# Kernel tuning notes

Measured on AMD Instinct MI355X. Metric: run time of the kernel, lower is better.

The kernel has to match this reference:

```python
import jax
import jax.numpy as jnp
import numpy as np
from jax import lax

STD = 1.0          # prior gaussian std
LAMBDA_2 = 0.1
LAMBDA_3 = 1000.0
MAX_ITER = 20
TOL = 1e-05
DIM = 512
SEQ = 4096


def mahalanobis_dist(P, Q, M):
    # dist[i,j] = (P_i - Q_j)^T M (P_i - Q_j)
    pMp = jnp.einsum('id,de,ie->i', P, M, P)          # [m]
    qMq = jnp.einsum('jd,de,je->j', Q, M, Q)          # [n]
    cross = P @ (M + M.T) @ Q.T                        # [m,n]
    return pMp[:, None] + qMq[None, :] - cross


def sinkhorn_iterative(K, alpha, beta, max_iter=MAX_ITER, tol=TOL):
    # Faithful replication of the torch loop (check at iter%20==1 or iter==max_iter).
    ainvK = K / alpha
    KT = K.T

    def check(u, v, it):
        v2 = beta / (KT @ u)
        u2 = 1.0 / (ainvK @ v2)
        crit = jnp.max(jnp.abs(jnp.sum(jnp.abs(v2 * (KT @ u2) - beta), axis=0)))  # inf-norm
        return u2, v2, it + 1, jnp.abs(crit) < tol

    def cond(state):
        _, _, it, done = state
        return (it < max_iter) & (~done)

    def body(state):
        u, v, it, done = state
        u = 1.0 / (ainvK @ (beta / (KT @ u)))
        it = it + 1
        do_check = ((it % 20) == 1) | (it == max_iter)
        return lax.cond(do_check,
                        lambda: check(u, v, it),
                        lambda: (u, v, it, done))

    u0 = alpha
    v0 = jnp.zeros_like(beta)
    u, v, _, _ = lax.while_loop(cond, body,
                                (u0, v0, jnp.asarray(0, jnp.int32), jnp.asarray(False)))
    return u, v


def W_M(P, Q, M):
    m, n = P.shape[0], Q.shape[0]
    dtype = P.dtype
    dist = mahalanobis_dist(P, Q, M)                                  # [m,n]
    alpha = (jnp.arange(1, m + 1, dtype=dtype) / m)[:, None]          # [m,1]
    beta = (jnp.arange(1, n + 1, dtype=dtype) / n)[:, None]           # [n,1]
    rel = alpha - beta.T                                              # [m,n]
    denom = jnp.sqrt(1.0 / n**2 + 1.0 / m**2)
    prior = (1.0 / (STD * np.sqrt(2.0 * np.pi))) * jnp.exp(
        -(jnp.abs(rel) / denom) ** 2 / (2.0 * STD**2))
    K = prior * jnp.exp(-(dist - LAMBDA_2 / (rel**2 + 1.0)) / LAMBDA_3)
    Kng = lax.stop_gradient(K)                                        # torch computed K under no_grad
    u, v = sinkhorn_iterative(Kng, alpha, beta)
    F = lax.stop_gradient(u * Kng * v.T)                              # detached transport plan
    return jnp.sum(F * dist)


def setup_inputs() -> dict:
    key = jax.random.key(0)
    kP, kQ, kR, kS, kM = jax.random.split(key, 5)
    P = jax.random.normal(kP, (SEQ, DIM), dtype=jnp.float32)
    Q = jax.random.normal(kQ, (SEQ, DIM), dtype=jnp.float32)
    R = jax.random.normal(kR, (SEQ, DIM), dtype=jnp.float32)
    S = jax.random.normal(kS, (SEQ, DIM), dtype=jnp.float32)
    M = jax.random.normal(kM, (DIM, DIM), dtype=jnp.float32)          # learned metric parameter
    return {"P": P, "Q": Q, "R": R, "S": S, "M": M}


def reference(P, Q, R, S, M):
    return W_M(P, Q, M) - W_M(R, S, M)
```

## Files before the change

### kernel.cpp

```cpp
#include <hip/hip_runtime.h>
#include <hip/hip_bf16.h>
#include <math.h>

#define SEQ   4096
#define DIM   512
#define BW    24
#define NDIAG 49
#define TW    56
#define VSTR  4608
#define VOFF  256
#define INV_N (1.0f/4096.0f)

#define OFF_KT   0
#define SZ_KT    (2*SEQ*TW/2)
#define OFF_KC   (OFF_KT + SZ_KT)
#define SZ_KC    (2*SEQ*TW/2)
#define OFF_DT   (OFF_KC + SZ_KC)
#define SZ_DT    (2*SEQ*TW)
#define OFF_VEC  (OFF_DT + SZ_DT)
#define SZ_VEC   (6*VSTR)
#define OFF_PX   (OFF_VEC + SZ_VEC)
#define SZ_PX    (4*SEQ)
#define OFF_SC   (OFF_PX + SZ_PX)
#define SZ_SC    16
#define OFF_BBF  (OFF_SC + SZ_SC)
#define SZ_BBF   (DIM*DIM/2)
#define OFF_QBF  (OFF_BBF + SZ_BBF)
#define SZ_QBF   (2*SEQ*DIM/2)
#define OFF_GBF  (OFF_QBF + SZ_QBF)
#define SZ_GBF   (2*SEQ*DIM/2)
#define WS_FLOATS (OFF_GBF + SZ_GBF)

typedef __attribute__((ext_vector_type(8))) short short8;
typedef __attribute__((ext_vector_type(8))) unsigned short ushort8;
typedef __attribute__((ext_vector_type(4))) float f32x4;

__device__ __forceinline__ ushort f2bfh(float f) {
    __hip_bfloat16 h = __float2bfloat16(f);
    return *reinterpret_cast<ushort*>(&h);
}
__device__ __forceinline__ float bf2f(ushort u) {
    union { unsigned u; float f; } w; w.u = ((unsigned)u) << 16; return w.f;
}

__device__ __forceinline__ void gload16(void* lds, const void* g) {
    __builtin_amdgcn_global_load_lds(
        (const __attribute__((address_space(1))) unsigned int*)g,
        (__attribute__((address_space(3))) unsigned int*)lds,
        16, 0, 0);
}

#define ZQUADS (OFF_BBF/4)
#define ZBLK   ((ZQUADS + 255)/256)
#define BBLK   1024
#define CBLK   4096
#define PREP_BLOCKS (ZBLK + BBLK + CBLK)

__global__ void kprep(const float* __restrict__ M, const float* __restrict__ Q,
                      const float* __restrict__ S, float* __restrict__ ws) {
    int b = blockIdx.x, tid = threadIdx.x;
    if (b < ZBLK) {
        int q = b*256 + tid;
        if (q < ZQUADS)
            *reinterpret_cast<float4*>(&ws[(size_t)q*4]) = (float4){0.f,0.f,0.f,0.f};
    } else if (b < ZBLK + BBLK) {
        int idx = (b - ZBLK)*256 + tid;
        int d = idx >> 9, e = idx & 511;
        ((ushort*)(ws + OFF_BBF))[idx] = f2bfh(M[d*DIM + e] + M[e*DIM + d]);
    } else {
        int cb = b - (ZBLK + BBLK);
        int g = cb >> 11;
        const float* src = g ? S : Q;
        size_t idx = ((size_t)(cb & 2047)*256 + tid)*4;
        float4 v = *reinterpret_cast<const float4*>(&src[idx]);
        ushort4 o;
        o.x = f2bfh(v.x); o.y = f2bfh(v.y); o.z = f2bfh(v.z); o.w = f2bfh(v.w);
        *reinterpret_cast<ushort4*>(((ushort*)(ws + OFF_QBF)) + (size_t)g*SEQ*DIM + idx) = o;
    }
}

__launch_bounds__(256, 2)
__global__ void kgemm4(const float* __restrict__ P, const float* __restrict__ R,
                       const ushort* __restrict__ Qbf, const ushort* __restrict__ Bbf,
                       ushort* __restrict__ GBbf, float* __restrict__ pX) {
    int z = blockIdx.z;
    int abf = z & 1;
    const float*  Xf = (z == 0) ? P : R;
    const ushort* Xh = Qbf + (size_t)(z >> 1)*SEQ*DIM;
    int i0 = blockIdx.x * 128;
    int j0 = blockIdx.y * 128;
    __shared__ float  As[2*128*32];
    __shared__ ushort Bs[2*128*32];
    int tid = threadIdx.x, wv = tid >> 6, l = tid & 63;
    int h = l >> 4, lr = l & 15;
    int wrow = (wv >> 1)*64, wcol = (wv & 1)*64;

    auto stageB = [&](int buf, int kc) {
        #pragma unroll
        for (int s2 = 0; s2 < 2; ++s2) {
            int seg = wv*2 + s2;
            int col = seg*16 + (l >> 2);
            int cs = (l & 3) ^ (col & 3);
            gload16((char*)Bs + (size_t)buf*8192 + seg*1024,
                    &Bbf[(size_t)(j0+col)*DIM + kc + cs*8]);
        }
    };
    auto stageAf = [&](int buf, int kc) {
        #pragma unroll
        for (int s2 = 0; s2 < 4; ++s2) {
            int seg = wv*4 + s2;
            int row = seg*8 + (l >> 3);
            int cs = (l & 7) ^ (row & 7);
            gload16((char*)As + (size_t)buf*16384 + seg*1024,
                    &Xf[(size_t)(i0+row)*DIM + kc + cs*4]);
        }
    };
    auto stageAh = [&](int buf, int kc) {
        #pragma unroll
        for (int s2 = 0; s2 < 2; ++s2) {
            int seg = wv*2 + s2;
            gload16((char*)As + (size_t)buf*8192 + seg*1024,
                    &Xh[(size_t)(i0 + (seg&1)*64 + l)*DIM + kc + (seg>>1)*8]);
        }
    };

    f32x4 acc[4][4];
    #pragma unroll
    for (int a = 0; a < 4; ++a)
        #pragma unroll
        for (int b = 0; b < 4; ++b) acc[a][b] = (f32x4){0.f,0.f,0.f,0.f};

    if (abf) stageAh(0, 0); else stageAf(0, 0);
    stageB(0, 0);
    __syncthreads();
    for (int t = 0; t < 16; ++t) {
        int cur = t & 1;
        if (t < 15) {
            if (abf) stageAh(cur ^ 1, (t+1)*32); else stageAf(cur ^ 1, (t+1)*32);
            stageB(cur ^ 1, (t+1)*32);
        }
        short8 a8[4], b8[4];
        if (abf) {
            #pragma unroll
            for (int rt = 0; rt < 4; ++rt) {
                int row = wrow + rt*16 + lr;
                a8[rt] = *reinterpret_cast<const short8*>(
                    (const char*)As + (size_t)cur*8192 + h*2048 + row*16);
            }
        } else {
            #pragma unroll
            for (int rt = 0; rt < 4; ++rt) {
                int row = wrow + rt*16 + lr;
                const char* base = (const char*)As + (size_t)cur*16384 + row*128;
                int c1 = (2*h)     ^ (row & 7);
                int c2 = (2*h + 1) ^ (row & 7);
                float4 fa = *reinterpret_cast<const float4*>(base + c1*16);
                float4 fb = *reinterpret_cast<const float4*>(base + c2*16);
                short8 tt;
                tt[0]=(short)f2bfh(fa.x); tt[1]=(short)f2bfh(fa.y);
                tt[2]=(short)f2bfh(fa.z); tt[3]=(short)f2bfh(fa.w);
                tt[4]=(short)f2bfh(fb.x); tt[5]=(short)f2bfh(fb.y);
                tt[6]=(short)f2bfh(fb.z); tt[7]=(short)f2bfh(fb.w);
                a8[rt] = tt;
            }
        }
        #pragma unroll
        for (int ct = 0; ct < 4; ++ct) {
            int col = wcol + ct*16 + lr;
            int c = h ^ (col & 3);
            b8[ct] = *reinterpret_cast<const short8*>(
                (const char*)Bs + (size_t)cur*8192 + col*64 + c*16);
        }
        #pragma unroll
        for (int rt = 0; rt < 4; ++rt)
            #pragma unroll
            for (int ct = 0; ct < 4; ++ct)
                acc[rt][ct] = __builtin_amdgcn_mfma_f32_16x16x32_bf16(a8[rt], b8[ct], acc[rt][ct], 0, 0, 0);
        __syncthreads();
    }

    #pragma unroll
    for (int rt = 0; rt < 4; ++rt) {
        #pragma unroll
        for (int r = 0; r < 4; ++r) {
            int row = wrow + rt*16 + h*4 + r;
            float v = 0.f;
            #pragma unroll
            for (int ct = 0; ct < 4; ++ct) {
                int col = wcol + ct*16 + lr;
                float cv = acc[rt][ct][r];
                float xv;
                if (abf) xv = bf2f(Xh[(size_t)(i0+row)*DIM + j0 + col]);
                else     xv = Xf[(size_t)(i0+row)*DIM + j0 + col];
                v = fmaf(cv, xv, v);
                if (!abf)
                    GBbf[((size_t)((z>>1)*SEQ + i0 + row))*DIM + j0 + col] = f2bfh(cv);
            }
            v += __shfl_xor(v, 1); v += __shfl_xor(v, 2);
            v += __shfl_xor(v, 4); v += __shfl_xor(v, 8);
            if (lr == 0) atomicAdd(&pX[(size_t)z*SEQ + i0 + row], 0.5f*v);
        }
    }
}

__launch_bounds__(64)
__global__ void kband3(const ushort* __restrict__ GBbf, const ushort* __restrict__ Qbf,
                       const float* __restrict__ pX,
                       ushort* __restrict__ Ktb, ushort* __restrict__ Kcb,
                       float* __restrict__ Dt) {
    int g = blockIdx.y;
    int i0 = blockIdx.x * 16;
    int l = threadIdx.x;
    const ushort* A = GBbf + (size_t)g*SEQ*DIM;
    const ushort* Y = Qbf  + (size_t)g*SEQ*DIM;
    const float* pM = pX + (size_t)(2*g)*SEQ;
    const float* qM = pX + (size_t)(2*g+1)*SEQ;
    int jbase = i0 - BW;
    int arow = i0 + (l & 15);
    int koff = (l >> 4) * 8;
    int jcl[4];
    #pragma unroll
    for (int ct = 0; ct < 4; ++ct) {
        int j = jbase + ct*16 + (l & 15);
        jcl[ct] = min(max(j, 0), SEQ-1);
    }
    f32x4 acc[4];
    #pragma unroll
    for (int ct = 0; ct < 4; ++ct) acc[ct] = (f32x4){0.f,0.f,0.f,0.f};
    #pragma unroll
    for (int ks = 0; ks < 16; ++ks) {
        int kk = ks*32 + koff;
        short8 af = *reinterpret_cast<const short8*>(&A[(size_t)arow*DIM + kk]);
        #pragma unroll
        for (int ct = 0; ct < 4; ++ct) {
            short8 bf = *reinterpret_cast<const short8*>(&Y[(size_t)jcl[ct]*DIM + kk]);
            acc[ct] = __builtin_amdgcn_mfma_f32_16x16x32_bf16(af, bf, acc[ct], 0, 0, 0);
        }
    }
    #pragma unroll
    for (int ct = 0; ct < 4; ++ct) {
        #pragma unroll
        for (int r = 0; r < 4; ++r) {
            int i = i0 + (l >> 4)*4 + r;
            int j = jbase + ct*16 + (l & 15);
            int d = j - i;
            if (d >= -BW && d <= BW && j >= 0 && j < SEQ) {
                float dist = pM[i] + qM[j] - acc[ct][r];
                float fd = (float)d;
                float rel = fd * (1.0f/4096.0f);
                float cd = -0.91893853f - 0.25f*fd*fd + 1e-4f/(rel*rel + 1.0f);
                float Kv = expf(cd - dist*1e-3f);
                ushort kvu = f2bfh(Kv);
                Ktb[((size_t)g*SEQ + i)*TW + (d + BW)] = kvu;
                Kcb[((size_t)g*SEQ + j)*TW + (BW - d)] = kvu;
                Dt [((size_t)g*SEQ + i)*TW + (d + BW)] = dist;
            }
        }
    }
}

#define SR3  64
#define SB3  416
__launch_bounds__(256)
__global__ void ksink3(const ushort* __restrict__ Ktb, const ushort* __restrict__ Kcb,
                       float* __restrict__ vecs, float* __restrict__ sc,
                       int nsteps, int firstT, int alphaInit,
                       int vstep, int ustep, int cstep, int gated, int inSlot, int outSlot) {
    int g = blockIdx.y;
    if (gated && sc[g] < 1e-5f) return;
    int r0 = blockIdx.x * SR3;
    int ext = 24 * nsteps;
    __shared__ float bufA[SB3];
    __shared__ float bufB[SB3];
    __shared__ float vsave[SB3];
    __shared__ float red[256];
    float* bin = bufA;
    float* bout = bufB;
    int base = r0 - ext;
    int range0 = SR3 + 2*ext;
    const float* vin = vecs + (size_t)(inSlot*2 + g)*VSTR;
    for (int L = threadIdx.x; L < SB3; L += 256) {
        int gr = base + L;
        float v = 0.f;
        if (L < range0 && gr >= 0 && gr < SEQ)
            v = alphaInit ? (gr+1)*INV_N : vin[VOFF + gr];
        bufA[L] = v;
        bufB[L] = 0.f;
    }
    __syncthreads();
    float critloc = 0.f;
    for (int m = 0; m < nsteps; ++m) {
        int e = 24*(nsteps - 1 - m);
        int lo = ext - e;
        int cnt = SR3 + 2*e;
        int typeT = firstT ^ (m & 1);
        const ushort* tap0 = (typeT ? Kcb : Ktb) + (size_t)g*SEQ*TW;
        for (int t = threadIdx.x; t < cnt; t += 256) {
            int L = lo + t;
            int gr = base + L;
            float o = 0.f;
            if (gr >= 0 && gr < SEQ) {
                const ushort* tap = tap0 + (size_t)gr*TW;
                float s = 0.f;
                #pragma unroll
                for (int c = 0; c < 7; ++c) {
                    ushort8 k8 = *reinterpret_cast<const ushort8*>(tap + c*8);
                    #pragma unroll
                    for (int ee = 0; ee < 8; ++ee)
                        s = fmaf(bf2f(k8[ee]), bin[L + c*8 + ee - BW], s);
                }
                float ab = (gr+1)*INV_N;
                o = ab / s;
                if (m == vstep) {
                    vecs[(size_t)(4 + g)*VSTR + VOFF + gr] = o;
                    if (cstep >= 0) vsave[L] = o;
                }
                if (m == ustep)
                    vecs[(size_t)g*VSTR + VOFF + gr] = o;
                if (m == cstep)
                    critloc += fabsf(vsave[L]*s - ab);
            }
            bout[L] = o;
        }
        __syncthreads();
        float* tmp = bin; bin = bout; bout = tmp;
    }
    if (threadIdx.x < SR3) {
        int gr = r0 + threadIdx.x;
        vecs[(size_t)(outSlot*2 + g)*VSTR + VOFF + gr] = bin[ext + threadIdx.x];
    }
    if (cstep >= 0) {
        red[threadIdx.x] = critloc;
        __syncthreads();
        for (int s = 128; s > 0; s >>= 1) {
            if (threadIdx.x < s) red[threadIdx.x] += red[threadIdx.x + s];
            __syncthreads();
        }
        if (threadIdx.x == 0) atomicAdd(&sc[g], red[0]);
    }
}

__launch_bounds__(256)
__global__ void kfinal(const ushort* __restrict__ Ktb, const float* __restrict__ Dt,
                       const float* __restrict__ vecs, float* __restrict__ sc) {
    int g = blockIdx.y;
    int i = blockIdx.x * 256 + threadIdx.x;
    const ushort* kt = Ktb + ((size_t)g*SEQ + i)*TW;
    const float*  dt = Dt  + ((size_t)g*SEQ + i)*TW;
    const float* u = vecs + (size_t)g*VSTR + VOFF;
    const float* v = vecs + (size_t)(4 + g)*VSTR + VOFF;
    float ss = 0.f;
    #pragma unroll
    for (int c = 0; c < 7; ++c) {
        ushort8 k8 = *reinterpret_cast<const ushort8*>(kt + c*8);
        #pragma unroll
        for (int ee = 0; ee < 8; ++ee) {
            int t = c*8 + ee;
            ss += bf2f(k8[ee]) * dt[t] * v[i + t - BW];
        }
    }
    ss *= u[i];
    __shared__ float red[256];
    red[threadIdx.x] = ss;
    __syncthreads();
    for (int s = 128; s > 0; s >>= 1) {
        if (threadIdx.x < s) red[threadIdx.x] += red[threadIdx.x + s];
        __syncthreads();
    }
    if (threadIdx.x == 0) atomicAdd(&sc[2+g], red[0]);
}

__global__ void kout(const float* __restrict__ sc, float* __restrict__ out) {
    out[0] = sc[2] - sc[3];
}

extern "C" void kernel_launch(void* const* d_in, const int* in_sizes, int n_in,
                              void* d_out, int out_size, void* d_ws, size_t ws_size,
                              hipStream_t stream) {
    const float* P = (const float*)d_in[0];
    const float* Q = (const float*)d_in[1];
    const float* R = (const float*)d_in[2];
    const float* S = (const float*)d_in[3];
    const float* M = (const float*)d_in[4];
    float* ws = (float*)d_ws;
    if (ws_size < (size_t)WS_FLOATS * sizeof(float)) return;

    ushort* Ktb = (ushort*)(ws + OFF_KT);
    ushort* Kcb = (ushort*)(ws + OFF_KC);
    float*  Dt  = ws + OFF_DT;
    float*  vec = ws + OFF_VEC;
    float*  pX  = ws + OFF_PX;
    float*  sc  = ws + OFF_SC;
    ushort* Bbf = (ushort*)(ws + OFF_BBF);
    ushort* Qbf = (ushort*)(ws + OFF_QBF);
    ushort* GBbf= (ushort*)(ws + OFF_GBF);

    kprep <<<dim3(PREP_BLOCKS), dim3(256), 0, stream>>>(M, Q, S, ws);
    kgemm4<<<dim3(32, 4, 4),    dim3(256), 0, stream>>>(P, R, Qbf, Bbf, GBbf, pX);
    kband3<<<dim3(256, 2),      dim3(64),  0, stream>>>(GBbf, Qbf, pX, Ktb, Kcb, Dt);

    ksink3<<<dim3(64,2), dim3(256), 0, stream>>>(Ktb, Kcb, vec, sc,  5, 1, 1,  2,  3,  4, 0, 0, 1);
    ksink3<<<dim3(64,2), dim3(256), 0, stream>>>(Ktb, Kcb, vec, sc,  6, 0, 0, -1, -1, -1, 1, 1, 1);
    ksink3<<<dim3(64,2), dim3(256), 0, stream>>>(Ktb, Kcb, vec, sc,  6, 0, 0, -1, -1, -1, 1, 1, 1);
    ksink3<<<dim3(64,2), dim3(256), 0, stream>>>(Ktb, Kcb, vec, sc,  6, 0, 0, -1, -1, -1, 1, 1, 1);
    ksink3<<<dim3(64,2), dim3(256), 0, stream>>>(Ktb, Kcb, vec, sc,  6, 0, 0, -1, -1, -1, 1, 1, 1);
    ksink3<<<dim3(64,2), dim3(256), 0, stream>>>(Ktb, Kcb, vec, sc,  6, 0, 0, -1, -1, -1, 1, 1, 1);
    ksink3<<<dim3(64,2), dim3(256), 0, stream>>>(Ktb, Kcb, vec, sc,  7, 0, 0,  5, -1, -1, 1, 1, 0);

    kfinal<<<dim3(16,2), dim3(256), 0, stream>>>(Ktb, Dt, vec, sc);
    kout  <<<dim3(1),    dim3(1),   0, stream>>>(sc, (float*)d_out);
}
```

Baseline: 159.6 us.

## Pre-convert all inputs to bf16, store band kernel in fp32, shrink sinkhorn tiles

P and R are now converted to bf16 in the prep kernel alongside Q and S, so one GEMM kernel with a single bf16 A path replaces the mixed fp32/bf16 path, and its occupancy hint rises to 4 blocks. The banded K matrices move from bf16 to fp32 storage, doubling their memory traffic in the sinkhorn and final kernels but dropping the bf16 rounding of K. Sinkhorn row tiles are halved so twice as many blocks launch, and the division is replaced by a hardware reciprocal. The extra prep pass adds memory traffic in exchange for a simpler GEMM inner loop.

Measured after the change: 160.3 us. Within noise of the previous version (+0.4%).

```diff
diff --git a/kernel.cpp b/kernel.cpp
--- a/kernel.cpp
+++ b/kernel.cpp
@@ -12,12 +12,10 @@
 #define INV_N (1.0f/4096.0f)
 
 #define OFF_KT   0
-#define SZ_KT    (2*SEQ*TW/2)
-#define OFF_KC   (OFF_KT + SZ_KT)
-#define SZ_KC    (2*SEQ*TW/2)
-#define OFF_DT   (OFF_KC + SZ_KC)
-#define SZ_DT    (2*SEQ*TW)
-#define OFF_VEC  (OFF_DT + SZ_DT)
+#define SZ_T     (2*SEQ*TW)
+#define OFF_KC   (OFF_KT + SZ_T)
+#define OFF_DT   (OFF_KC + SZ_T)
+#define OFF_VEC  (OFF_DT + SZ_T)
 #define SZ_VEC   (6*VSTR)
 #define OFF_PX   (OFF_VEC + SZ_VEC)
 #define SZ_PX    (4*SEQ)
@@ -25,14 +23,13 @@
 #define SZ_SC    16
 #define OFF_BBF  (OFF_SC + SZ_SC)
 #define SZ_BBF   (DIM*DIM/2)
-#define OFF_QBF  (OFF_BBF + SZ_BBF)
-#define SZ_QBF   (2*SEQ*DIM/2)
-#define OFF_GBF  (OFF_QBF + SZ_QBF)
+#define OFF_XBF  (OFF_BBF + SZ_BBF)
+#define SZ_XBF   (4*SEQ*DIM/2)
+#define OFF_GBF  (OFF_XBF + SZ_XBF)
 #define SZ_GBF   (2*SEQ*DIM/2)
 #define WS_FLOATS (OFF_GBF + SZ_GBF)
 
 typedef __attribute__((ext_vector_type(8))) short short8;
-typedef __attribute__((ext_vector_type(8))) unsigned short ushort8;
 typedef __attribute__((ext_vector_type(4))) float f32x4;
 
 __device__ __forceinline__ ushort f2bfh(float f) {
@@ -53,11 +50,12 @@
 #define ZQUADS (OFF_BBF/4)
 #define ZBLK   ((ZQUADS + 255)/256)
 #define BBLK   1024
-#define CBLK   4096
+#define CBLK   8192
 #define PREP_BLOCKS (ZBLK + BBLK + CBLK)
 
-__global__ void kprep(const float* __restrict__ M, const float* __restrict__ Q,
-                      const float* __restrict__ S, float* __restrict__ ws) {
+__global__ void kprep(const float* __restrict__ P, const float* __restrict__ Q,
+                      const float* __restrict__ R, const float* __restrict__ S,
+                      const float* __restrict__ M, float* __restrict__ ws) {
     int b = blockIdx.x, tid = threadIdx.x;
     if (b < ZBLK) {
         int q = b*256 + tid;
@@ -69,32 +67,37 @@
         ((ushort*)(ws + OFF_BBF))[idx] = f2bfh(M[d*DIM + e] + M[e*DIM + d]);
     } else {
         int cb = b - (ZBLK + BBLK);
-        int g = cb >> 11;
-        const float* src = g ? S : Q;
+        int z = cb >> 11;
+        const float* src = (z==0) ? P : (z==1) ? Q : (z==2) ? R : S;
         size_t idx = ((size_t)(cb & 2047)*256 + tid)*4;
         float4 v = *reinterpret_cast<const float4*>(&src[idx]);
         ushort4 o;
         o.x = f2bfh(v.x); o.y = f2bfh(v.y); o.z = f2bfh(v.z); o.w = f2bfh(v.w);
-        *reinterpret_cast<ushort4*>(((ushort*)(ws + OFF_QBF)) + (size_t)g*SEQ*DIM + idx) = o;
-    }
-}
-
-__launch_bounds__(256, 2)
-__global__ void kgemm4(const float* __restrict__ P, const float* __restrict__ R,
-                       const ushort* __restrict__ Qbf, const ushort* __restrict__ Bbf,
+        *reinterpret_cast<ushort4*>(((ushort*)(ws + OFF_XBF)) + (size_t)z*SEQ*DIM + idx) = o;
+    }
+}
+
+__launch_bounds__(256, 4)
+__global__ void kgemm5(const ushort* __restrict__ Xbf, const ushort* __restrict__ Bbf,
                        ushort* __restrict__ GBbf, float* __restrict__ pX) {
     int z = blockIdx.z;
-    int abf = z & 1;
-    const float*  Xf = (z == 0) ? P : R;
-    const ushort* Xh = Qbf + (size_t)(z >> 1)*SEQ*DIM;
+    const ushort* Xh = Xbf + (size_t)z*SEQ*DIM;
     int i0 = blockIdx.x * 128;
     int j0 = blockIdx.y * 128;
-    __shared__ float  As[2*128*32];
-    __shared__ ushort Bs[2*128*32];
+    __shared__ ushort As[2*4096];
+    __shared__ ushort Bs[2*4096];
     int tid = threadIdx.x, wv = tid >> 6, l = tid & 63;
     int h = l >> 4, lr = l & 15;
     int wrow = (wv >> 1)*64, wcol = (wv & 1)*64;
 
+    auto stageA = [&](int buf, int kc) {
+        #pragma unroll
+        for (int s2 = 0; s2 < 2; ++s2) {
+            int seg = wv*2 + s2;
+            gload16((char*)As + (size_t)buf*8192 + seg*1024,
+                    &Xh[(size_t)(i0 + (seg&1)*64 + l)*DIM + kc + (seg>>1)*8]);
+        }
+    };
     auto stageB = [&](int buf, int kc) {
         #pragma unroll
         for (int s2 = 0; s2 < 2; ++s2) {
@@ -105,24 +108,6 @@
                     &Bbf[(size_t)(j0+col)*DIM + kc + cs*8]);
         }
     };
-    auto stageAf = [&](int buf, int kc) {
-        #pragma unroll
-        for (int s2 = 0; s2 < 4; ++s2) {
-            int seg = wv*4 + s2;
-            int row = seg*8 + (l >> 3);
-            int cs = (l & 7) ^ (row & 7);
-            gload16((char*)As + (size_t)buf*16384 + seg*1024,
-                    &Xf[(size_t)(i0+row)*DIM + kc + cs*4]);
-        }
-    };
-    auto stageAh = [&](int buf, int kc) {
-        #pragma unroll
-        for (int s2 = 0; s2 < 2; ++s2) {
-            int seg = wv*2 + s2;
-            gload16((char*)As + (size_t)buf*8192 + seg*1024,
-                    &Xh[(size_t)(i0 + (seg&1)*64 + l)*DIM + kc + (seg>>1)*8]);
-        }
-    };
 
     f32x4 acc[4][4];
     #pragma unroll
@@ -130,39 +115,17 @@
         #pragma unroll
         for (int b = 0; b < 4; ++b) acc[a][b] = (f32x4){0.f,0.f,0.f,0.f};
 
-    if (abf) stageAh(0, 0); else stageAf(0, 0);
-    stageB(0, 0);
+    stageA(0, 0); stageB(0, 0);
     __syncthreads();
     for (int t = 0; t < 16; ++t) {
         int cur = t & 1;
-        if (t < 15) {
-            if (abf) stageAh(cur ^ 1, (t+1)*32); else stageAf(cur ^ 1, (t+1)*32);
-            stageB(cur ^ 1, (t+1)*32);
-        }
+        if (t < 15) { stageA(cur ^ 1, (t+1)*32); stageB(cur ^ 1, (t+1)*32); }
         short8 a8[4], b8[4];
-        if (abf) {
-            #pragma unroll
-            for (int rt = 0; rt < 4; ++rt) {
-                int row = wrow + rt*16 + lr;
-                a8[rt] = *reinterpret_cast<const short8*>(
-                    (const char*)As + (size_t)cur*8192 + h*2048 + row*16);
-            }
-        } else {
-            #pragma unroll
-            for (int rt = 0; rt < 4; ++rt) {
-                int row = wrow + rt*16 + lr;
-                const char* base = (const char*)As + (size_t)cur*16384 + row*128;
-                int c1 = (2*h)     ^ (row & 7);
-                int c2 = (2*h + 1) ^ (row & 7);
-                float4 fa = *reinterpret_cast<const float4*>(base + c1*16);
-                float4 fb = *reinterpret_cast<const float4*>(base + c2*16);
-                short8 tt;
-                tt[0]=(short)f2bfh(fa.x); tt[1]=(short)f2bfh(fa.y);
-                tt[2]=(short)f2bfh(fa.z); tt[3]=(short)f2bfh(fa.w);
-                tt[4]=(short)f2bfh(fb.x); tt[5]=(short)f2bfh(fb.y);
-                tt[6]=(short)f2bfh(fb.z); tt[7]=(short)f2bfh(fb.w);
-                a8[rt] = tt;
-            }
+        #pragma unroll
+        for (int rt = 0; rt < 4; ++rt) {
+            int row = wrow + rt*16 + lr;
+            a8[rt] = *reinterpret_cast<const short8*>(
+                (const char*)As + (size_t)cur*8192 + h*2048 + row*16);
         }
         #pragma unroll
         for (int ct = 0; ct < 4; ++ct) {
@@ -189,11 +152,9 @@
             for (int ct = 0; ct < 4; ++ct) {
                 int col = wcol + ct*16 + lr;
                 float cv = acc[rt][ct][r];
-                float xv;
-                if (abf) xv = bf2f(Xh[(size_t)(i0+row)*DIM + j0 + col]);
-                else     xv = Xf[(size_t)(i0+row)*DIM + j0 + col];
+                float xv = bf2f(Xh[(size_t)(i0+row)*DIM + j0 + col]);
                 v = fmaf(cv, xv, v);
-                if (!abf)
+                if ((z & 1) == 0)
                     GBbf[((size_t)((z>>1)*SEQ + i0 + row))*DIM + j0 + col] = f2bfh(cv);
             }
             v += __shfl_xor(v, 1); v += __shfl_xor(v, 2);
@@ -204,15 +165,15 @@
 }
 
 __launch_bounds__(64)
-__global__ void kband3(const ushort* __restrict__ GBbf, const ushort* __restrict__ Qbf,
+__global__ void kband3(const ushort* __restrict__ GBbf, const ushort* __restrict__ Xbf,
                        const float* __restrict__ pX,
-                       ushort* __restrict__ Ktb, ushort* __restrict__ Kcb,
+                       float* __restrict__ Ktb, float* __restrict__ Kcb,
                        float* __restrict__ Dt) {
     int g = blockIdx.y;
     int i0 = blockIdx.x * 16;
     int l = threadIdx.x;
     const ushort* A = GBbf + (size_t)g*SEQ*DIM;
-    const ushort* Y = Qbf  + (size_t)g*SEQ*DIM;
+    const ushort* Y = Xbf + (size_t)(1 + 2*g)*SEQ*DIM;
     const float* pM = pX + (size_t)(2*g)*SEQ;
     const float* qM = pX + (size_t)(2*g+1)*SEQ;
     int jbase = i0 - BW;
@@ -250,19 +211,18 @@
                 float rel = fd * (1.0f/4096.0f);
                 float cd = -0.91893853f - 0.25f*fd*fd + 1e-4f/(rel*rel + 1.0f);
                 float Kv = expf(cd - dist*1e-3f);
-                ushort kvu = f2bfh(Kv);
-                Ktb[((size_t)g*SEQ + i)*TW + (d + BW)] = kvu;
-                Kcb[((size_t)g*SEQ + j)*TW + (BW - d)] = kvu;
+                Ktb[((size_t)g*SEQ + i)*TW + (d + BW)] = Kv;
+                Kcb[((size_t)g*SEQ + j)*TW + (BW - d)] = Kv;
                 Dt [((size_t)g*SEQ + i)*TW + (d + BW)] = dist;
             }
         }
     }
 }
 
-#define SR3  64
-#define SB3  416
+#define SR3  32
+#define SB3  384
 __launch_bounds__(256)
-__global__ void ksink3(const ushort* __restrict__ Ktb, const ushort* __restrict__ Kcb,
+__global__ void ksink3(const float* __restrict__ Ktb, const float* __restrict__ Kcb,
                        float* __restrict__ vecs, float* __restrict__ sc,
                        int nsteps, int firstT, int alphaInit,
                        int vstep, int ustep, int cstep, int gated, int inSlot, int outSlot) {
@@ -294,23 +254,24 @@
         int lo = ext - e;
         int cnt = SR3 + 2*e;
         int typeT = firstT ^ (m & 1);
-        const ushort* tap0 = (typeT ? Kcb : Ktb) + (size_t)g*SEQ*TW;
+        const float* tap0 = (typeT ? Kcb : Ktb) + (size_t)g*SEQ*TW;
         for (int t = threadIdx.x; t < cnt; t += 256) {
             int L = lo + t;
             int gr = base + L;
             float o = 0.f;
             if (gr >= 0 && gr < SEQ) {
-                const ushort* tap = tap0 + (size_t)gr*TW;
+                const float* tap = tap0 + (size_t)gr*TW;
                 float s = 0.f;
                 #pragma unroll
-                for (int c = 0; c < 7; ++c) {
-                    ushort8 k8 = *reinterpret_cast<const ushort8*>(tap + c*8);
-                    #pragma unroll
-                    for (int ee = 0; ee < 8; ++ee)
-                        s = fmaf(bf2f(k8[ee]), bin[L + c*8 + ee - BW], s);
+                for (int c = 0; c < 14; ++c) {
+                    float4 k4 = *reinterpret_cast<const float4*>(tap + c*4);
+                    s = fmaf(k4.x, bin[L + c*4 + 0 - BW], s);
+                    s = fmaf(k4.y, bin[L + c*4 + 1 - BW], s);
+                    s = fmaf(k4.z, bin[L + c*4 + 2 - BW], s);
+                    s = fmaf(k4.w, bin[L + c*4 + 3 - BW], s);
                 }
                 float ab = (gr+1)*INV_N;
-                o = ab / s;
+                o = ab * __builtin_amdgcn_rcpf(s);
                 if (m == vstep) {
                     vecs[(size_t)(4 + g)*VSTR + VOFF + gr] = o;
                     if (cstep >= 0) vsave[L] = o;
@@ -341,23 +302,23 @@
 }
 
 __launch_bounds__(256)
-__global__ void kfinal(const ushort* __restrict__ Ktb, const float* __restrict__ Dt,
+__global__ void kfinal(const float* __restrict__ Ktb, const float* __restrict__ Dt,
                        const float* __restrict__ vecs, float* __restrict__ sc) {
     int g = blockIdx.y;
     int i = blockIdx.x * 256 + threadIdx.x;
-    const ushort* kt = Ktb + ((size_t)g*SEQ + i)*TW;
-    const float*  dt = Dt  + ((size_t)g*SEQ + i)*TW;
+    const float* kt = Ktb + ((size_t)g*SEQ + i)*TW;
+    const float* dt = Dt  + ((size_t)g*SEQ + i)*TW;
     const float* u = vecs + (size_t)g*VSTR + VOFF;
     const float* v = vecs + (size_t)(4 + g)*VSTR + VOFF;
     float ss = 0.f;
     #pragma unroll
-    for (int c = 0; c < 7; ++c) {
-        ushort8 k8 = *reinterpret_cast<const ushort8*>(kt + c*8);
-        #pragma unroll
-        for (int ee = 0; ee < 8; ++ee) {
-            int t = c*8 + ee;
-            ss += bf2f(k8[ee]) * dt[t] * v[i + t - BW];
-        }
+    for (int c = 0; c < 14; ++c) {
+        float4 k4 = *reinterpret_cast<const float4*>(kt + c*4);
+        float4 d4 = *reinterpret_cast<const float4*>(dt + c*4);
+        ss += k4.x * d4.x * v[i + c*4 + 0 - BW];
+        ss += k4.y * d4.y * v[i + c*4 + 1 - BW];
+        ss += k4.z * d4.z * v[i + c*4 + 2 - BW];
+        ss += k4.w * d4.w * v[i + c*4 + 3 - BW];
     }
     ss *= u[i];
     __shared__ float red[256];
@@ -385,27 +346,27 @@
     float* ws = (float*)d_ws;
     if (ws_size < (size_t)WS_FLOATS * sizeof(float)) return;
 
-    ushort* Ktb = (ushort*)(ws + OFF_KT);
-    ushort* Kcb = (ushort*)(ws + OFF_KC);
+    float*  Ktb = ws + OFF_KT;
+    float*  Kcb = ws + OFF_KC;
     float*  Dt  = ws + OFF_DT;
     float*  vec = ws + OFF_VEC;
     float*  pX  = ws + OFF_PX;
     float*  sc  = ws + OFF_SC;
     ushort* Bbf = (ushort*)(ws + OFF_BBF);
-    ushort* Qbf = (ushort*)(ws + OFF_QBF);
+    ushort* Xbf = (ushort*)(ws + OFF_XBF);
     ushort* GBbf= (ushort*)(ws + OFF_GBF);
 
-    kprep <<<dim3(PREP_BLOCKS), dim3(256), 0, stream>>>(M, Q, S, ws);
-    kgemm4<<<dim3(32, 4, 4),    dim3(256), 0, stream>>>(P, R, Qbf, Bbf, GBbf, pX);
-    kband3<<<dim3(256, 2),      dim3(64),  0, stream>>>(GBbf, Qbf, pX, Ktb, Kcb, Dt);
-
-    ksink3<<<dim3(64,2), dim3(256), 0, stream>>>(Ktb, Kcb, vec, sc,  5, 1, 1,  2,  3,  4, 0, 0, 1);
-    ksink3<<<dim3(64,2), dim3(256), 0, stream>>>(Ktb, Kcb, vec, sc,  6, 0, 0, -1, -1, -1, 1, 1, 1);
-    ksink3<<<dim3(64,2), dim3(256), 0, stream>>>(Ktb, Kcb, vec, sc,  6, 0, 0, -1, -1, -1, 1, 1, 1);
-    ksink3<<<dim3(64,2), dim3(256), 0, stream>>>(Ktb, Kcb, vec, sc,  6, 0, 0, -1, -1, -1, 1, 1, 1);
-    ksink3<<<dim3(64,2), dim3(256), 0, stream>>>(Ktb, Kcb, vec, sc,  6, 0, 0, -1, -1, -1, 1, 1, 1);
-    ksink3<<<dim3(64,2), dim3(256), 0, stream>>>(Ktb, Kcb, vec, sc,  6, 0, 0, -1, -1, -1, 1, 1, 1);
-    ksink3<<<dim3(64,2), dim3(256), 0, stream>>>(Ktb, Kcb, vec, sc,  7, 0, 0,  5, -1, -1, 1, 1, 0);
+    kprep <<<dim3(PREP_BLOCKS), dim3(256), 0, stream>>>(P, Q, R, S, M, ws);
+    kgemm5<<<dim3(32, 4, 4),    dim3(256), 0, stream>>>(Xbf, Bbf, GBbf, pX);
+    kband3<<<dim3(256, 2),      dim3(64),  0, stream>>>(GBbf, Xbf, pX, Ktb, Kcb, Dt);
+
+    ksink3<<<dim3(128,2), dim3(256), 0, stream>>>(Ktb, Kcb, vec, sc,  5, 1, 1,  2,  3,  4, 0, 0, 1);
+    ksink3<<<dim3(128,2), dim3(256), 0, stream>>>(Ktb, Kcb, vec, sc,  6, 0, 0, -1, -1, -1, 1, 1, 1);
+    ksink3<<<dim3(128,2), dim3(256), 0, stream>>>(Ktb, Kcb, vec, sc,  6, 0, 0, -1, -1, -1, 1, 1, 1);
+    ksink3<<<dim3(128,2), dim3(256), 0, stream>>>(Ktb, Kcb, vec, sc,  6, 0, 0, -1, -1, -1, 1, 1, 1);
+    ksink3<<<dim3(128,2), dim3(256), 0, stream>>>(Ktb, Kcb, vec, sc,  6, 0, 0, -1, -1, -1, 1, 1, 1);
+    ksink3<<<dim3(128,2), dim3(256), 0, stream>>>(Ktb, Kcb, vec, sc,  6, 0, 0, -1, -1, -1, 1, 1, 1);
+    ksink3<<<dim3(128,2), dim3(256), 0, stream>>>(Ktb, Kcb, vec, sc,  7, 0, 0,  5, -1, -1, 1, 1, 0);
 
     kfinal<<<dim3(16,2), dim3(256), 0, stream>>>(Ktb, Dt, vec, sc);
     kout  <<<dim3(1),    dim3(1),   0, stream>>>(sc, (float*)d_out);
```
